# Kernel tuning notes

Measured on AMD Instinct MI355X. Metric: run time of the kernel, lower is better.

Reference implementation:

```python
import jax, jax.numpy as jnp
import numpy as np

DIM = 512

def setup_inputs() -> dict:
    key = jax.random.key(0)
    ks = jax.random.split(key, 7)
    S = 8192
    scale = 1.0 / np.sqrt(DIM)
    x = jax.random.normal(ks[0], (S, DIM), dtype=jnp.float32)
    # torch.nn.Linear params: weight [out, in], bias [out]
    Wq = jax.random.uniform(ks[1], (DIM, DIM), jnp.float32, -scale, scale)
    bq = jax.random.uniform(ks[2], (DIM,), jnp.float32, -scale, scale)
    Wk = jax.random.uniform(ks[3], (DIM, DIM), jnp.float32, -scale, scale)
    bk = jax.random.uniform(ks[4], (DIM,), jnp.float32, -scale, scale)
    Wv = jax.random.uniform(ks[5], (DIM, DIM), jnp.float32, -scale, scale)
    bv = jax.random.uniform(ks[6], (DIM,), jnp.float32, -scale, scale)
    return {"x": x, "Wq": Wq, "bq": bq, "Wk": Wk, "bk": bk, "Wv": Wv, "bv": bv}

def reference(x, Wq, bq, Wk, bk, Wv, bv):
    S = x.shape[0]
    q = x @ Wq.T + bq  # [S, D]
    k = x @ Wk.T + bk
    v = x @ Wv.T + bv
    scores = (q @ k.T) / jnp.sqrt(jnp.asarray(DIM, x.dtype))  # [S, S]
    causal = jnp.tril(jnp.ones((S, S), dtype=bool))  # keep lower triangle incl. diag
    scores = jnp.where(causal, scores, -jnp.inf)
    attn_weights = jax.nn.softmax(scores, axis=-1)
    output = attn_weights @ v  # [S, D]
    return (output, attn_weights)
```

## Files before the change

kernel.cpp:

```cpp
#include <hip/hip_runtime.h>
#include <hip/hip_bf16.h>
#include <stdint.h>

#define S 8192
#define D 512
#define SCALE 0.044194173824159216f
#define KZ 4
#define NEG_BIG -1e30f

typedef __attribute__((ext_vector_type(8))) short short8;
typedef __attribute__((ext_vector_type(4))) float f32x4;

__device__ inline unsigned short f32_to_bf16(float f) {
    union { float f; uint32_t u; } v; v.f = f;
    uint32_t u = v.u;
    uint32_t r = (u + 0x7FFFu + ((u >> 16) & 1u)) >> 16;
    return (unsigned short)r;
}

__device__ inline uint2 pack4(float4 v) {
    uint2 p;
    p.x = (uint32_t)f32_to_bf16(v.x) | ((uint32_t)f32_to_bf16(v.y) << 16);
    p.y = (uint32_t)f32_to_bf16(v.z) | ((uint32_t)f32_to_bf16(v.w) << 16);
    return p;
}

__device__ inline void gload16(const void* g, void* l) {
    __builtin_amdgcn_global_load_lds(
        (const __attribute__((address_space(1))) unsigned int*)g,
        (__attribute__((address_space(3))) unsigned int*)l, 16, 0, 0);
}

__device__ inline void stage_g2l(const short* __restrict__ src, int ld, short* dst, int t) {
    int w = t >> 6, l = t & 63;
    int lr = l >> 2, lc = (l & 3) * 8;
#pragma unroll
    for (int j = 0; j < 2; j++) {
        int row = (w << 5) + (j << 4) + lr;
        gload16(src + (size_t)row * ld + lc, dst + (w << 10) + (j << 9));
    }
}

__device__ inline void mfma_tile(const short* As, const short* Bs,
                                 f32x4 acc[4][4], int wr, int wc, int lane) {
    int rl = lane & 15;
    int kg = lane >> 4;
    short8 a[4], b[4];
#pragma unroll
    for (int m = 0; m < 4; m++)
        a[m] = *reinterpret_cast<const short8*>(&As[(wr * 64 + m * 16 + rl) * 32 + kg * 8]);
#pragma unroll
    for (int n = 0; n < 4; n++)
        b[n] = *reinterpret_cast<const short8*>(&Bs[(wc * 64 + n * 16 + rl) * 32 + kg * 8]);
#pragma unroll
    for (int m = 0; m < 4; m++)
#pragma unroll
        for (int n = 0; n < 4; n++)
            acc[m][n] = __builtin_amdgcn_mfma_f32_16x16x32_bf16(a[m], b[n], acc[m][n], 0, 0, 0);
}

__global__ __launch_bounds__(256) void k_convert(
    const float* __restrict__ x, const float* __restrict__ Wq,
    const float* __restrict__ Wk, const float* __restrict__ Wv,
    short* __restrict__ xb, short* __restrict__ Wb) {
    size_t i4 = (size_t)blockIdx.x * 256 + threadIdx.x;
    const size_t XN4 = (size_t)S * D / 4;
    if (i4 < XN4) {
        float4 v = reinterpret_cast<const float4*>(x)[i4];
        reinterpret_cast<uint2*>(xb)[i4] = pack4(v);
    } else {
        size_t j4 = i4 - XN4;
        size_t w = j4 >> 16;
        size_t rem = j4 & 65535;
        const float* src = (w == 0) ? Wq : ((w == 1) ? Wk : Wv);
        float4 v = reinterpret_cast<const float4*>(src)[rem];
        reinterpret_cast<uint2*>(Wb)[j4] = pack4(v);
    }
}

__global__ __launch_bounds__(256) void k_qkv(
    const short* __restrict__ xb, const short* __restrict__ Wb,
    const float* __restrict__ bq, const float* __restrict__ bk,
    const float* __restrict__ bv, short* __restrict__ QKV) {
    __shared__ __align__(16) short As[128 * 32], Bs[128 * 32];
    int which = blockIdx.z;
    const short* W = Wb + (size_t)which * D * D;
    const float* bias = (which == 0) ? bq : ((which == 1) ? bk : bv);
    short* out = QKV + (size_t)which * S * D;
    int r0 = blockIdx.x * 128, c0 = blockIdx.y * 128;
    int t = threadIdx.x, lane = t & 63, w = t >> 6, wr = w >> 1, wc = w & 1;
    f32x4 acc[4][4];
#pragma unroll
    for (int m = 0; m < 4; m++)
#pragma unroll
        for (int n = 0; n < 4; n++)
#pragma unroll
            for (int j = 0; j < 4; j++) acc[m][n][j] = 0.0f;

    for (int kk = 0; kk < D; kk += 32) {
        __syncthreads();
        stage_g2l(xb + (size_t)r0 * D + kk, D, As, t);
        stage_g2l(W + (size_t)c0 * D + kk, D, Bs, t);
        __syncthreads();
        mfma_tile(As, Bs, acc, wr, wc, lane);
    }
    int rg = lane >> 4, cl = lane & 15;
#pragma unroll
    for (int m = 0; m < 4; m++)
#pragma unroll
        for (int n = 0; n < 4; n++) {
            int col = c0 + wc * 64 + n * 16 + cl;
            float b = bias[col];
#pragma unroll
            for (int j = 0; j < 4; j++) {
                int row = r0 + wr * 64 + m * 16 + rg * 4 + j;
                out[(size_t)row * D + col] = (short)f32_to_bf16(acc[m][n][j] + b);
            }
        }
}

__global__ __launch_bounds__(256) void k_transpose(const short* __restrict__ V,
                                                   short* __restrict__ Vt) {
    __shared__ short tile[64][65];
    int r0 = blockIdx.x * 64;
    int c0 = blockIdx.y * 64;
    int t = threadIdx.x;
#pragma unroll
    for (int j = 0; j < 16; j++) {
        int idx = t + j * 256;
        int r = idx >> 6, c = idx & 63;
        tile[r][c] = V[(size_t)(r0 + r) * D + c0 + c];
    }
    __syncthreads();
#pragma unroll
    for (int j = 0; j < 16; j++) {
        int idx = t + j * 256;
        int rr = idx >> 6, cc = idx & 63;
        Vt[(size_t)(c0 + rr) * S + r0 + cc] = tile[cc][rr];
    }
}

__global__ __launch_bounds__(256) void k_scores(const short* __restrict__ Qb,
                                                const short* __restrict__ Kb,
                                                float* __restrict__ raw,
                                                float* __restrict__ attn,
                                                float* __restrict__ pm,
                                                float* __restrict__ pl) {
    int bj = blockIdx.x, bi = blockIdx.y;
    int r0 = bi * 128, c0 = bj * 128;
    int t = threadIdx.x;
    if (bj > bi) {
#pragma unroll
        for (int j = 0; j < 16; j++) {
            int c = t + j * 256;
            int r = c >> 5;
            int c4 = (c & 31) * 4;
            *reinterpret_cast<float4*>(&attn[(size_t)(r0 + r) * S + c0 + c4]) =
                make_float4(0.f, 0.f, 0.f, 0.f);
        }
        return;
    }
    __shared__ __align__(16) short As[128 * 32], Bs[128 * 32];
    __shared__ float wred[2][128], wsum[2][128];
    int lane = t & 63, w = t >> 6, wr = w >> 1, wc = w & 1;
    f32x4 acc[4][4];
#pragma unroll
    for (int m = 0; m < 4; m++)
#pragma unroll
        for (int n = 0; n < 4; n++)
#pragma unroll
            for (int j = 0; j < 4; j++) acc[m][n][j] = 0.0f;

    for (int kk = 0; kk < D; kk += 32) {
        __syncthreads();
        stage_g2l(Qb + (size_t)r0 * D + kk, D, As, t);
        stage_g2l(Kb + (size_t)c0 * D + kk, D, Bs, t);
        __syncthreads();
        mfma_tile(As, Bs, acc, wr, wc, lane);
    }
    int rg = lane >> 4, cl = lane & 15;
    bool diag = (bi == bj);
#pragma unroll
    for (int m = 0; m < 4; m++)
#pragma unroll
        for (int n = 0; n < 4; n++)
#pragma unroll
            for (int jj = 0; jj < 4; jj++) {
                int row = wr * 64 + m * 16 + rg * 4 + jj;
                int col = wc * 64 + n * 16 + cl;
                float v = acc[m][n][jj] * SCALE;
                if (diag && col > row) v = NEG_BIG;
                acc[m][n][jj] = v;
            }
#pragma unroll
    for (int m = 0; m < 4; m++)
#pragma unroll
        for (int jj = 0; jj < 4; jj++) {
            float x = fmaxf(fmaxf(acc[m][0][jj], acc[m][1][jj]),
                            fmaxf(acc[m][2][jj], acc[m][3][jj]));
#pragma unroll
            for (int o = 1; o < 16; o <<= 1) x = fmaxf(x, __shfl_xor(x, o, 64));
            if (cl == 0) wred[wc][wr * 64 + m * 16 + rg * 4 + jj] = x;
        }
    __syncthreads();
#pragma unroll
    for (int m = 0; m < 4; m++)
#pragma unroll
        for (int jj = 0; jj < 4; jj++) {
            int rloc = wr * 64 + m * 16 + rg * 4 + jj;
            float mr = fmaxf(wred[0][rloc], wred[1][rloc]);
            float sse = __expf(acc[m][0][jj] - mr) + __expf(acc[m][1][jj] - mr) +
                        __expf(acc[m][2][jj] - mr) + __expf(acc[m][3][jj] - mr);
#pragma unroll
            for (int o = 1; o < 16; o <<= 1) sse += __shfl_xor(sse, o, 64);
            if (cl == 0) wsum[wc][rloc] = sse;
        }
#pragma unroll
    for (int m = 0; m < 4; m++)
#pragma unroll
        for (int n = 0; n < 4; n++) {
            int col = c0 + wc * 64 + n * 16 + cl;
#pragma unroll
            for (int jj = 0; jj < 4; jj++) {
                int row = r0 + wr * 64 + m * 16 + rg * 4 + jj;
                raw[(size_t)row * S + col] = acc[m][n][jj];
            }
        }
    __syncthreads();
    if (t < 128) {
        float mr = fmaxf(wred[0][t], wred[1][t]);
        pm[(size_t)bj * S + r0 + t] = mr;
        pl[(size_t)bj * S + r0 + t] = wsum[0][t] + wsum[1][t];
    }
}

__global__ __launch_bounds__(256) void k_combine(const float* __restrict__ pm,
                                                 const float* __restrict__ pl,
                                                 float* __restrict__ M,
                                                 float* __restrict__ Li) {
    int row = blockIdx.x * 256 + threadIdx.x;
    int nt = (row >> 7) + 1;
    float m = -3e38f;
    for (int j = 0; j < nt; j++) m = fmaxf(m, pm[(size_t)j * S + row]);
    float l = 0.f;
    for (int j = 0; j < nt; j++) l += pl[(size_t)j * S + row] * __expf(pm[(size_t)j * S + row] - m);
    M[row] = m;
    Li[row] = 1.0f / l;
}

__global__ __launch_bounds__(512) void k_pvnorm(const float* __restrict__ raw,
                                                const short* __restrict__ Vt,
                                                const float* __restrict__ M,
                                                const float* __restrict__ Li,
                                                float* __restrict__ attn,
                                                float* __restrict__ out) {
    int idx = blockIdx.x;
    int panel = 63 - (idx & 63);
    int rest = idx >> 6;
    int bn = rest & 1;
    int kz = rest >> 1;
    int r0 = panel * 128;
    int t = threadIdx.x;
    int nst = (panel + 1) * 4;
    int per = (nst + KZ - 1) / KZ;
    int st0 = kz * per, st1 = min(nst, st0 + per);
    if (st0 >= st1) return;
    __shared__ __align__(16) short As[128 * 32];
    __shared__ __align__(16) short Bs[256 * 32];
    __shared__ float Ml[128], Ll[128];
    if (t < 128) { Ml[t] = M[r0 + t]; Ll[t] = Li[r0 + t]; }
    int lane = t & 63, w = t >> 6, wr = w >> 2, wc = w & 3;
    f32x4 acc[4][4];
#pragma unroll
    for (int m = 0; m < 4; m++)
#pragma unroll
        for (int n = 0; n < 4; n++)
#pragma unroll
            for (int j = 0; j < 4; j++) acc[m][n][j] = 0.0f;

    const short* vbase = Vt + (size_t)(bn * 256) * S;
    for (int st = st0; st < st1; ++st) {
        int kk = st * 32;
        __syncthreads();
#pragma unroll
        for (int j = 0; j < 2; j++) {
            int c = t + j * 512;
            int r = c >> 3, kc = (c & 7) * 4;
            float4 v = *reinterpret_cast<const float4*>(&raw[(size_t)(r0 + r) * S + kk + kc]);
            float mlr = Ml[r], llr = Ll[r];
            float4 p;
            p.x = __expf(v.x - mlr) * llr;
            p.y = __expf(v.y - mlr) * llr;
            p.z = __expf(v.z - mlr) * llr;
            p.w = __expf(v.w - mlr) * llr;
            if (bn == 0)
                *reinterpret_cast<float4*>(&attn[(size_t)(r0 + r) * S + kk + kc]) = p;
            *reinterpret_cast<uint2*>(&As[r * 32 + kc]) = pack4(p);
        }
        stage_g2l(vbase + kk, S, Bs, t);
        __syncthreads();
        mfma_tile(As, Bs, acc, wr, wc, lane);
    }
    int rg = lane >> 4, cl = lane & 15;
#pragma unroll
    for (int m = 0; m < 4; m++)
#pragma unroll
        for (int n = 0; n < 4; n++) {
            int col = bn * 256 + wc * 64 + n * 16 + cl;
#pragma unroll
            for (int jj = 0; jj < 4; jj++) {
                int row = r0 + wr * 64 + m * 16 + rg * 4 + jj;
                atomicAdd(&out[(size_t)row * D + col], acc[m][n][jj]);
            }
        }
}

extern "C" void kernel_launch(void* const* d_in, const int* in_sizes, int n_in,
                              void* d_out, int out_size, void* d_ws, size_t ws_size,
                              hipStream_t stream) {
    const float* x  = (const float*)d_in[0];
    const float* Wq = (const float*)d_in[1];
    const float* bq = (const float*)d_in[2];
    const float* Wk = (const float*)d_in[3];
    const float* bk = (const float*)d_in[4];
    const float* Wv = (const float*)d_in[5];
    const float* bv = (const float*)d_in[6];
    float* out  = (float*)d_out;
    float* attn = out + (size_t)S * D;

    short* xb  = (short*)d_ws;
    short* Wb  = xb + (size_t)S * D;
    short* QKV = Wb + (size_t)3 * D * D;
    short* Vt  = QKV + (size_t)3 * S * D;
    float* raw = (float*)(Vt + (size_t)S * D);
    float* pm  = raw + (size_t)S * S;
    float* pl  = pm + (size_t)64 * S;
    float* M   = pl + (size_t)64 * S;
    float* Li  = M + S;

    const short* Qb = QKV;
    const short* Kb = QKV + (size_t)S * D;
    const short* Vb = QKV + (size_t)2 * S * D;

    {
        size_t total4 = (size_t)S * D / 4 + (size_t)3 * D * D / 4;
        k_convert<<<dim3((unsigned)(total4 / 256)), 256, 0, stream>>>(x, Wq, Wk, Wv, xb, Wb);
    }
    k_qkv<<<dim3(S / 128, D / 128, 3), 256, 0, stream>>>(xb, Wb, bq, bk, bv, QKV);
    k_transpose<<<dim3(S / 64, D / 64), 256, 0, stream>>>(Vb, Vt);
    k_scores<<<dim3(S / 128, S / 128), 256, 0, stream>>>(Qb, Kb, raw, attn, pm, pl);
    k_combine<<<dim3(S / 256), 256, 0, stream>>>(pm, pl, M, Li);
    hipMemsetAsync(d_out, 0, (size_t)S * D * sizeof(float), stream);
    k_pvnorm<<<dim3(2 * 64 * KZ), 512, 0, stream>>>(raw, Vt, M, Li, attn, out);
}
```

Baseline: 588.2 us.

## Store unnormalized bf16 exp scores, drop max pass, triangular grids for scores and PV

```diff
diff --git a/kernel.cpp b/kernel.cpp
--- a/kernel.cpp
+++ b/kernel.cpp
@@ -5,8 +5,7 @@
 #define S 8192
 #define D 512
 #define SCALE 0.044194173824159216f
-#define KZ 4
-#define NEG_BIG -1e30f
+#define CH 32
 
 typedef __attribute__((ext_vector_type(8))) short short8;
 typedef __attribute__((ext_vector_type(4))) float f32x4;
@@ -14,10 +13,11 @@
 __device__ inline unsigned short f32_to_bf16(float f) {
     union { float f; uint32_t u; } v; v.f = f;
     uint32_t u = v.u;
-    uint32_t r = (u + 0x7FFFu + ((u >> 16) & 1u)) >> 16;
-    return (unsigned short)r;
-}
-
+    return (unsigned short)((u + 0x7FFFu + ((u >> 16) & 1u)) >> 16);
+}
+__device__ inline float bf2f(unsigned short u) {
+    union { float f; uint32_t v; } x; x.v = (uint32_t)u << 16; return x.f;
+}
 __device__ inline uint2 pack4(float4 v) {
     uint2 p;
     p.x = (uint32_t)f32_to_bf16(v.x) | ((uint32_t)f32_to_bf16(v.y) << 16);
@@ -31,32 +31,34 @@
         (__attribute__((address_space(3))) unsigned int*)l, 16, 0, 0);
 }
 
-__device__ inline void stage_g2l(const short* __restrict__ src, int ld, short* dst, int t) {
-    int w = t >> 6, l = t & 63;
-    int lr = l >> 2, lc = (l & 3) * 8;
-#pragma unroll
-    for (int j = 0; j < 2; j++) {
-        int row = (w << 5) + (j << 4) + lr;
-        gload16(src + (size_t)row * ld + lc, dst + (w << 10) + (j << 9));
-    }
-}
-
-__device__ inline void mfma_tile(const short* As, const short* Bs,
-                                 f32x4 acc[4][4], int wr, int wc, int lane) {
-    int rl = lane & 15;
-    int kg = lane >> 4;
-    short8 a[4], b[4];
-#pragma unroll
-    for (int m = 0; m < 4; m++)
-        a[m] = *reinterpret_cast<const short8*>(&As[(wr * 64 + m * 16 + rl) * 32 + kg * 8]);
-#pragma unroll
-    for (int n = 0; n < 4; n++)
-        b[n] = *reinterpret_cast<const short8*>(&Bs[(wc * 64 + n * 16 + rl) * 32 + kg * 8]);
-#pragma unroll
-    for (int m = 0; m < 4; m++)
-#pragma unroll
-        for (int n = 0; n < 4; n++)
-            acc[m][n] = __builtin_amdgcn_mfma_f32_16x16x32_bf16(a[m], b[n], acc[m][n], 0, 0, 0);
+__device__ inline void stage128x64(const short* __restrict__ src, int ld,
+                                   short* dst, int w, int lane) {
+#pragma unroll
+    for (int j = 0; j < 4; j++) {
+        int c = (w * 4 + j) * 64 + lane;
+        int row = c >> 3, q = c & 7;
+        gload16(src + (size_t)row * ld + q * 8, dst + (size_t)(w * 4 + j) * 512);
+    }
+}
+
+__device__ inline void mfma_step64(const short* As, const short* Bs,
+                                   f32x4 acc[4][4], int wr, int wc, int lane) {
+    int rl = lane & 15, kg = lane >> 4;
+#pragma unroll
+    for (int kk0 = 0; kk0 < 64; kk0 += 32) {
+        short8 a[4], b[4];
+#pragma unroll
+        for (int m = 0; m < 4; m++)
+            a[m] = *reinterpret_cast<const short8*>(&As[(wr * 64 + m * 16 + rl) * 64 + kk0 + kg * 8]);
+#pragma unroll
+        for (int n = 0; n < 4; n++)
+            b[n] = *reinterpret_cast<const short8*>(&Bs[(wc * 64 + n * 16 + rl) * 64 + kk0 + kg * 8]);
+#pragma unroll
+        for (int m = 0; m < 4; m++)
+#pragma unroll
+            for (int n = 0; n < 4; n++)
+                acc[m][n] = __builtin_amdgcn_mfma_f32_16x16x32_bf16(a[m], b[n], acc[m][n], 0, 0, 0);
+    }
 }
 
 __global__ __launch_bounds__(256) void k_convert(
@@ -82,7 +84,9 @@
     const short* __restrict__ xb, const short* __restrict__ Wb,
     const float* __restrict__ bq, const float* __restrict__ bk,
     const float* __restrict__ bv, short* __restrict__ QKV) {
-    __shared__ __align__(16) short As[128 * 32], Bs[128 * 32];
+    __shared__ __align__(16) short smem[128 * 128];
+    short* As = smem;
+    short* Bs = smem + 128 * 64;
     int which = blockIdx.z;
     const short* W = Wb + (size_t)which * D * D;
     const float* bias = (which == 0) ? bq : ((which == 1) ? bk : bv);
@@ -97,26 +101,36 @@
 #pragma unroll
             for (int j = 0; j < 4; j++) acc[m][n][j] = 0.0f;
 
-    for (int kk = 0; kk < D; kk += 32) {
-        __syncthreads();
-        stage_g2l(xb + (size_t)r0 * D + kk, D, As, t);
-        stage_g2l(W + (size_t)c0 * D + kk, D, Bs, t);
-        __syncthreads();
-        mfma_tile(As, Bs, acc, wr, wc, lane);
-    }
+    for (int kk = 0; kk < D; kk += 64) {
+        __syncthreads();
+        stage128x64(xb + (size_t)r0 * D + kk, D, As, w, lane);
+        stage128x64(W + (size_t)c0 * D + kk, D, Bs, w, lane);
+        __syncthreads();
+        mfma_step64(As, Bs, acc, wr, wc, lane);
+    }
+    __syncthreads();
+    short* Es = smem;
     int rg = lane >> 4, cl = lane & 15;
 #pragma unroll
     for (int m = 0; m < 4; m++)
 #pragma unroll
         for (int n = 0; n < 4; n++) {
-            int col = c0 + wc * 64 + n * 16 + cl;
-            float b = bias[col];
-#pragma unroll
-            for (int j = 0; j < 4; j++) {
-                int row = r0 + wr * 64 + m * 16 + rg * 4 + j;
-                out[(size_t)row * D + col] = (short)f32_to_bf16(acc[m][n][j] + b);
+            int cloc = wc * 64 + n * 16 + cl;
+            float b = bias[c0 + cloc];
+#pragma unroll
+            for (int jj = 0; jj < 4; jj++) {
+                int rloc = wr * 64 + m * 16 + rg * 4 + jj;
+                Es[rloc * 128 + cloc] = (short)f32_to_bf16(acc[m][n][jj] + b);
             }
         }
+    __syncthreads();
+#pragma unroll
+    for (int j = 0; j < 8; j++) {
+        int c = t + j * 256;
+        int row = c >> 4, q = c & 15;
+        *reinterpret_cast<uint4*>(&out[(size_t)(r0 + row) * D + c0 + q * 8]) =
+            *reinterpret_cast<const uint4*>(&Es[row * 128 + q * 8]);
+    }
 }
 
 __global__ __launch_bounds__(256) void k_transpose(const short* __restrict__ V,
@@ -142,27 +156,19 @@
 
 __global__ __launch_bounds__(256) void k_scores(const short* __restrict__ Qb,
                                                 const short* __restrict__ Kb,
-                                                float* __restrict__ raw,
-                                                float* __restrict__ attn,
-                                                float* __restrict__ pm,
+                                                short* __restrict__ E,
                                                 float* __restrict__ pl) {
-    int bj = blockIdx.x, bi = blockIdx.y;
+    int bid = blockIdx.x;
+    int bi = 0, bj = 0;
+    { int c = 0;
+      for (int p = 0; p < 64; p++) { int n = p + 1;
+          if (bid < c + n) { bi = p; bj = bid - c; break; } c += n; } }
     int r0 = bi * 128, c0 = bj * 128;
-    int t = threadIdx.x;
-    if (bj > bi) {
-#pragma unroll
-        for (int j = 0; j < 16; j++) {
-            int c = t + j * 256;
-            int r = c >> 5;
-            int c4 = (c & 31) * 4;
-            *reinterpret_cast<float4*>(&attn[(size_t)(r0 + r) * S + c0 + c4]) =
-                make_float4(0.f, 0.f, 0.f, 0.f);
-        }
-        return;
-    }
-    __shared__ __align__(16) short As[128 * 32], Bs[128 * 32];
-    __shared__ float wred[2][128], wsum[2][128];
-    int lane = t & 63, w = t >> 6, wr = w >> 1, wc = w & 1;
+    __shared__ __align__(16) short smem[128 * 128];
+    short* As = smem;
+    short* Bs = smem + 128 * 64;
+    __shared__ float wsum[2][128];
+    int t = threadIdx.x, lane = t & 63, w = t >> 6, wr = w >> 1, wc = w & 1;
     f32x4 acc[4][4];
 #pragma unroll
     for (int m = 0; m < 4; m++)
@@ -171,104 +177,102 @@
 #pragma unroll
             for (int j = 0; j < 4; j++) acc[m][n][j] = 0.0f;
 
-    for (int kk = 0; kk < D; kk += 32) {
-        __syncthreads();
-        stage_g2l(Qb + (size_t)r0 * D + kk, D, As, t);
-        stage_g2l(Kb + (size_t)c0 * D + kk, D, Bs, t);
-        __syncthreads();
-        mfma_tile(As, Bs, acc, wr, wc, lane);
+    for (int kk = 0; kk < D; kk += 64) {
+        __syncthreads();
+        stage128x64(Qb + (size_t)r0 * D + kk, D, As, w, lane);
+        stage128x64(Kb + (size_t)c0 * D + kk, D, Bs, w, lane);
+        __syncthreads();
+        mfma_step64(As, Bs, acc, wr, wc, lane);
     }
     int rg = lane >> 4, cl = lane & 15;
     bool diag = (bi == bj);
 #pragma unroll
     for (int m = 0; m < 4; m++)
 #pragma unroll
-        for (int n = 0; n < 4; n++)
-#pragma unroll
-            for (int jj = 0; jj < 4; jj++) {
-                int row = wr * 64 + m * 16 + rg * 4 + jj;
-                int col = wc * 64 + n * 16 + cl;
-                float v = acc[m][n][jj] * SCALE;
-                if (diag && col > row) v = NEG_BIG;
-                acc[m][n][jj] = v;
-            }
-#pragma unroll
-    for (int m = 0; m < 4; m++)
-#pragma unroll
-        for (int jj = 0; jj < 4; jj++) {
-            float x = fmaxf(fmaxf(acc[m][0][jj], acc[m][1][jj]),
-                            fmaxf(acc[m][2][jj], acc[m][3][jj]));
-#pragma unroll
-            for (int o = 1; o < 16; o <<= 1) x = fmaxf(x, __shfl_xor(x, o, 64));
-            if (cl == 0) wred[wc][wr * 64 + m * 16 + rg * 4 + jj] = x;
-        }
-    __syncthreads();
-#pragma unroll
-    for (int m = 0; m < 4; m++)
-#pragma unroll
         for (int jj = 0; jj < 4; jj++) {
             int rloc = wr * 64 + m * 16 + rg * 4 + jj;
-            float mr = fmaxf(wred[0][rloc], wred[1][rloc]);
-            float sse = __expf(acc[m][0][jj] - mr) + __expf(acc[m][1][jj] - mr) +
-                        __expf(acc[m][2][jj] - mr) + __expf(acc[m][3][jj] - mr);
-#pragma unroll
-            for (int o = 1; o < 16; o <<= 1) sse += __shfl_xor(sse, o, 64);
-            if (cl == 0) wsum[wc][rloc] = sse;
-        }
+            float s4 = 0.f;
+#pragma unroll
+            for (int n = 0; n < 4; n++) {
+                int cloc = wc * 64 + n * 16 + cl;
+                float sv = acc[m][n][jj] * SCALE;
+                float e = (diag && cloc > rloc) ? 0.0f : __expf(sv);
+                acc[m][n][jj] = e;
+                s4 += e;
+            }
+#pragma unroll
+            for (int o = 1; o < 16; o <<= 1) s4 += __shfl_xor(s4, o, 64);
+            if (cl == 0) wsum[wc][rloc] = s4;
+        }
+    __syncthreads();
+    if (t < 128) pl[(size_t)bj * S + r0 + t] = wsum[0][t] + wsum[1][t];
+    short* Es = smem;
 #pragma unroll
     for (int m = 0; m < 4; m++)
 #pragma unroll
         for (int n = 0; n < 4; n++) {
-            int col = c0 + wc * 64 + n * 16 + cl;
+            int cloc = wc * 64 + n * 16 + cl;
 #pragma unroll
             for (int jj = 0; jj < 4; jj++) {
-                int row = r0 + wr * 64 + m * 16 + rg * 4 + jj;
-                raw[(size_t)row * S + col] = acc[m][n][jj];
+                int rloc = wr * 64 + m * 16 + rg * 4 + jj;
+                Es[rloc * 128 + cloc] = (short)f32_to_bf16(acc[m][n][jj]);
             }
         }
     __syncthreads();
-    if (t < 128) {
-        float mr = fmaxf(wred[0][t], wred[1][t]);
-        pm[(size_t)bj * S + r0 + t] = mr;
-        pl[(size_t)bj * S + r0 + t] = wsum[0][t] + wsum[1][t];
-    }
-}
-
-__global__ __launch_bounds__(256) void k_combine(const float* __restrict__ pm,
-                                                 const float* __restrict__ pl,
-                                                 float* __restrict__ M,
+#pragma unroll
+    for (int j = 0; j < 8; j++) {
+        int c = t + j * 256;
+        int row = c >> 4, q = c & 15;
+        *reinterpret_cast<uint4*>(&E[(size_t)(r0 + row) * S + c0 + q * 8]) =
+            *reinterpret_cast<const uint4*>(&Es[row * 128 + q * 8]);
+    }
+}
+
+__global__ __launch_bounds__(256) void k_combine(const float* __restrict__ pl,
                                                  float* __restrict__ Li) {
     int row = blockIdx.x * 256 + threadIdx.x;
     int nt = (row >> 7) + 1;
-    float m = -3e38f;
-    for (int j = 0; j < nt; j++) m = fmaxf(m, pm[(size_t)j * S + row]);
     float l = 0.f;
-    for (int j = 0; j < nt; j++) l += pl[(size_t)j * S + row] * __expf(pm[(size_t)j * S + row] - m);
-    M[row] = m;
+    for (int j = 0; j < nt; j++) l += pl[(size_t)j * S + row];
     Li[row] = 1.0f / l;
 }
 
-__global__ __launch_bounds__(512) void k_pvnorm(const float* __restrict__ raw,
-                                                const short* __restrict__ Vt,
-                                                const float* __restrict__ M,
-                                                const float* __restrict__ Li,
-                                                float* __restrict__ attn,
-                                                float* __restrict__ out) {
-    int idx = blockIdx.x;
-    int panel = 63 - (idx & 63);
-    int rest = idx >> 6;
-    int bn = rest & 1;
-    int kz = rest >> 1;
-    int r0 = panel * 128;
+__global__ __launch_bounds__(256) void k_zero(float* __restrict__ attn) {
+    int bid = blockIdx.x;
+    int bi = 0, bj = 0;
+    { int c = 0;
+      for (int p = 0; p < 63; p++) { int n = 63 - p;
+          if (bid < c + n) { bi = p; bj = p + 1 + (bid - c); break; } c += n; } }
     int t = threadIdx.x;
-    int nst = (panel + 1) * 4;
-    int per = (nst + KZ - 1) / KZ;
-    int st0 = kz * per, st1 = min(nst, st0 + per);
-    if (st0 >= st1) return;
+    float4 z = make_float4(0.f, 0.f, 0.f, 0.f);
+#pragma unroll
+    for (int j = 0; j < 16; j++) {
+        int c = t + j * 256;
+        int row = c >> 5, q = (c & 31) * 4;
+        *reinterpret_cast<float4*>(&attn[(size_t)(bi * 128 + row) * S + bj * 128 + q]) = z;
+    }
+}
+
+__global__ __launch_bounds__(512) void k_pv(const short* __restrict__ E,
+                                            const short* __restrict__ Vt,
+                                            const float* __restrict__ Li,
+                                            float* __restrict__ attn,
+                                            float* __restrict__ out) {
+    int bid = blockIdx.x;
+    int bn = bid & 1, bidx = bid >> 1;
+    int panel = 63, chunk = 0;
+    { int c = 0;
+      for (int p = 63; p >= 0; p--) {
+          int nb = (p + 8) >> 3;
+          if (bidx < c + nb) { panel = p; chunk = bidx - c; break; } c += nb; } }
+    int nst = 4 * (panel + 1);
+    int st0 = chunk * CH, st1 = min(nst, st0 + CH);
+    int r0 = panel * 128, c0 = bn * 256;
     __shared__ __align__(16) short As[128 * 32];
     __shared__ __align__(16) short Bs[256 * 32];
-    __shared__ float Ml[128], Ll[128];
-    if (t < 128) { Ml[t] = M[r0 + t]; Ll[t] = Li[r0 + t]; }
+    __shared__ float Lil[128];
+    int t = threadIdx.x;
+    if (t < 128) Lil[t] = Li[r0 + t];
     int lane = t & 63, w = t >> 6, wr = w >> 2, wc = w & 3;
     f32x4 acc[4][4];
 #pragma unroll
@@ -278,39 +282,57 @@
 #pragma unroll
             for (int j = 0; j < 4; j++) acc[m][n][j] = 0.0f;
 
-    const short* vbase = Vt + (size_t)(bn * 256) * S;
+    int arow = t >> 2, aq = t & 3;
+    bool wrHalf = (bn == 0) ? (arow < 64) : (arow >= 64);
+
     for (int st = st0; st < st1; ++st) {
         int kk = st * 32;
         __syncthreads();
+        { int c = w * 64 + lane; int row = c >> 2, q = c & 3;
+          gload16(E + (size_t)(r0 + row) * S + kk + q * 8, As + w * 512); }
 #pragma unroll
         for (int j = 0; j < 2; j++) {
-            int c = t + j * 512;
-            int r = c >> 3, kc = (c & 7) * 4;
-            float4 v = *reinterpret_cast<const float4*>(&raw[(size_t)(r0 + r) * S + kk + kc]);
-            float mlr = Ml[r], llr = Ll[r];
-            float4 p;
-            p.x = __expf(v.x - mlr) * llr;
-            p.y = __expf(v.y - mlr) * llr;
-            p.z = __expf(v.z - mlr) * llr;
-            p.w = __expf(v.w - mlr) * llr;
-            if (bn == 0)
-                *reinterpret_cast<float4*>(&attn[(size_t)(r0 + r) * S + kk + kc]) = p;
-            *reinterpret_cast<uint2*>(&As[r * 32 + kc]) = pack4(p);
-        }
-        stage_g2l(vbase + kk, S, Bs, t);
-        __syncthreads();
-        mfma_tile(As, Bs, acc, wr, wc, lane);
+            int c = (w * 2 + j) * 64 + lane; int row = c >> 2, q = c & 3;
+            gload16(Vt + (size_t)(c0 + row) * S + kk + q * 8, Bs + (size_t)(w * 2 + j) * 512);
+        }
+        if (wrHalf) {
+            const uint4 ev = *reinterpret_cast<const uint4*>(&E[(size_t)(r0 + arow) * S + kk + aq * 8]);
+            float li = Lil[arow];
+            const unsigned short* es = reinterpret_cast<const unsigned short*>(&ev);
+            float4 o0, o1;
+            o0.x = bf2f(es[0]) * li; o0.y = bf2f(es[1]) * li;
+            o0.z = bf2f(es[2]) * li; o0.w = bf2f(es[3]) * li;
+            o1.x = bf2f(es[4]) * li; o1.y = bf2f(es[5]) * li;
+            o1.z = bf2f(es[6]) * li; o1.w = bf2f(es[7]) * li;
+            float* ap = &attn[(size_t)(r0 + arow) * S + kk + aq * 8];
+            *reinterpret_cast<float4*>(ap) = o0;
+            *reinterpret_cast<float4*>(ap + 4) = o1;
+        }
+        __syncthreads();
+        int rl = lane & 15, kg = lane >> 4;
+        short8 a[4], b[4];
+#pragma unroll
+        for (int m = 0; m < 4; m++)
+            a[m] = *reinterpret_cast<const short8*>(&As[(wr * 64 + m * 16 + rl) * 32 + kg * 8]);
+#pragma unroll
+        for (int n = 0; n < 4; n++)
+            b[n] = *reinterpret_cast<const short8*>(&Bs[(wc * 64 + n * 16 + rl) * 32 + kg * 8]);
+#pragma unroll
+        for (int m = 0; m < 4; m++)
+#pragma unroll
+            for (int n = 0; n < 4; n++)
+                acc[m][n] = __builtin_amdgcn_mfma_f32_16x16x32_bf16(a[m], b[n], acc[m][n], 0, 0, 0);
     }
     int rg = lane >> 4, cl = lane & 15;
 #pragma unroll
     for (int m = 0; m < 4; m++)
 #pragma unroll
         for (int n = 0; n < 4; n++) {
-            int col = bn * 256 + wc * 64 + n * 16 + cl;
+            int col = c0 + wc * 64 + n * 16 + cl;
 #pragma unroll
             for (int jj = 0; jj < 4; jj++) {
-                int row = r0 + wr * 64 + m * 16 + rg * 4 + jj;
-                atomicAdd(&out[(size_t)row * D + col], acc[m][n][jj]);
+                int rloc = wr * 64 + m * 16 + rg * 4 + jj;
+                atomicAdd(&out[(size_t)(r0 + rloc) * D + col], acc[m][n][jj] * Lil[rloc]);
             }
         }
 }
@@ -332,11 +354,9 @@
     short* Wb  = xb + (size_t)S * D;
     short* QKV = Wb + (size_t)3 * D * D;
     short* Vt  = QKV + (size_t)3 * S * D;
-    float* raw = (float*)(Vt + (size_t)S * D);
-    float* pm  = raw + (size_t)S * S;
-    float* pl  = pm + (size_t)64 * S;
-    float* M   = pl + (size_t)64 * S;
-    float* Li  = M + S;
+    short* E   = Vt + (size_t)S * D;
+    float* pl  = (float*)(E + (size_t)S * S);
+    float* Li  = pl + (size_t)64 * S;
 
     const short* Qb = QKV;
     const short* Kb = QKV + (size_t)S * D;
@@ -348,8 +368,9 @@
     }
     k_qkv<<<dim3(S / 128, D / 128, 3), 256, 0, stream>>>(xb, Wb, bq, bk, bv, QKV);
     k_transpose<<<dim3(S / 64, D / 64), 256, 0, stream>>>(Vb, Vt);
-    k_scores<<<dim3(S / 128, S / 128), 256, 0, stream>>>(Qb, Kb, raw, attn, pm, pl);
-    k_combine<<<dim3(S / 256), 256, 0, stream>>>(pm, pl, M, Li);
+    k_scores<<<dim3(64 * 65 / 2), 256, 0, stream>>>(Qb, Kb, E, pl);
+    k_combine<<<dim3(S / 256), 256, 0, stream>>>(pl, Li);
+    k_zero<<<dim3(63 * 64 / 2), 256, 0, stream>>>(attn);
     hipMemsetAsync(d_out, 0, (size_t)S * D * sizeof(float), stream);
-    k_pvnorm<<<dim3(2 * 64 * KZ), 512, 0, stream>>>(raw, Vt, M, Li, attn, out);
-}
+    k_pv<<<dim3(2 * 288), 512, 0, stream>>>(E, Vt, Li, attn, out);
+}
```

After: 573.9 us. -2.4%, faster.
